# Optimization experiments

Hardware: AMD Instinct MI355X
Metric: run time of the kernel (lower is better)

The kernel has to match this reference:

```python
import jax, jax.numpy as jnp
import numpy as np
from jax import lax

IMG = 512            # image H = W
FH = FW = 32         # feature map spatial size
A = 9                # anchors per location (3 sizes x 3 ratios)
N = FH * FW * A      # total anchors = 9216
IOU_THR = 0.7
MIN_SCORE = 0.5
MIN_SIZE = 1e-3


def make_anchors():
    """Anchors in centroid format (cx, cy, w, h), ordered (H, W, A)."""
    stride = IMG / FH
    sizes = np.array([32.0, 64.0, 128.0])
    ratios = np.array([0.5, 1.0, 2.0])
    ws = (sizes[:, None] / np.sqrt(ratios)[None, :]).reshape(-1)  # (A,)
    hs = (sizes[:, None] * np.sqrt(ratios)[None, :]).reshape(-1)  # (A,)
    cx = (np.arange(FW) + 0.5) * stride
    cy = (np.arange(FH) + 0.5) * stride
    CX = np.broadcast_to(cx[None, :, None], (FH, FW, A))
    CY = np.broadcast_to(cy[:, None, None], (FH, FW, A))
    Wg = np.broadcast_to(ws[None, None, :], (FH, FW, A))
    Hg = np.broadcast_to(hs[None, None, :], (FH, FW, A))
    anc = np.stack([CX, CY, Wg, Hg], axis=-1).reshape(-1, 4)
    return jnp.asarray(anc, dtype=jnp.float32)


def pairwise_iou(b):
    # b: (N,4) corners x1,y1,x2,y2
    x1, y1, x2, y2 = b[:, 0], b[:, 1], b[:, 2], b[:, 3]
    area = (x2 - x1) * (y2 - y1)
    ix1 = jnp.maximum(x1[:, None], x1[None, :])
    iy1 = jnp.maximum(y1[:, None], y1[None, :])
    ix2 = jnp.minimum(x2[:, None], x2[None, :])
    iy2 = jnp.minimum(y2[:, None], y2[None, :])
    inter = jnp.maximum(ix2 - ix1, 0.0) * jnp.maximum(iy2 - iy1, 0.0)
    union = area[:, None] + area[None, :] - inter
    return inter / jnp.maximum(union, 1e-9)


def nms_keep(boxes, scores, valid):
    """Greedy NMS. Returns bool keep mask of shape (N,). Index decisions only."""
    s = jnp.where(valid, scores, -jnp.inf)
    order = jnp.argsort(-s)
    b = boxes[order]
    v = valid[order]
    ious = pairwise_iou(b)  # (N, N)
    idx = jnp.arange(N)

    def body(i, supp):
        keep_i = (~supp[i]) & v[i]
        return supp | (keep_i & (ious[i] > IOU_THR) & (idx > i))

    supp = lax.fori_loop(0, N, body, jnp.zeros(N, dtype=bool))
    keep_sorted = (~supp) & v
    return jnp.zeros(N, dtype=bool).at[order].set(keep_sorted)


def setup_inputs() -> dict:
    key = jax.random.key(0)
    ks = jax.random.split(key, 4)
    return {
        "feature_map": jax.random.normal(ks[0], (1, 256, FH, FW), jnp.float32),
        "conv1_w": jax.random.normal(ks[1], (512, 256, 3, 3), jnp.float32) * 0.02,
        "conv1_b": jnp.zeros((512,), jnp.float32),
        "conv2_w": jax.random.normal(ks[2], (A, 512), jnp.float32) * 0.01,
        "conv2_b": jnp.zeros((A,), jnp.float32),
        "conv3_w": jax.random.normal(ks[3], (4 * A, 512), jnp.float32) * 0.01,
        "conv3_b": jnp.zeros((4 * A,), jnp.float32),
    }


def reference(feature_map, conv1_w, conv1_b, conv2_w, conv2_b, conv3_w, conv3_b):
    anchors = make_anchors()  # (N,4) cx,cy,w,h

    # --- conv backbone head ---
    h = lax.conv_general_dilated(
        feature_map, conv1_w, (1, 1), "SAME",
        dimension_numbers=("NCHW", "OIHW", "NCHW"))
    h = jax.nn.relu(h + conv1_b[None, :, None, None])  # (1,512,H,W)

    scores = jax.nn.sigmoid(
        jnp.einsum("bchw,ac->bahw", h, conv2_w) + conv2_b[None, :, None, None])
    scores = scores.transpose(0, 2, 3, 1).reshape(-1)  # (N,) ordered (H,W,A)

    off = jnp.einsum("bchw,oc->bohw", h, conv3_w) + conv3_b[None, :, None, None]
    off = off.reshape(1, A, 4, FH, FW).transpose(0, 3, 4, 1, 2).reshape(-1, 4)

    acx, acy, aw, ah = anchors[:, 0], anchors[:, 1], anchors[:, 2], anchors[:, 3]
    cx = acx + off[:, 0] * aw
    cy = acy + off[:, 1] * ah
    bw = aw * jnp.exp(off[:, 2])
    bh = ah * jnp.exp(off[:, 3])
    boxes = jnp.stack([cx - bw / 2, cy - bh / 2, cx + bw / 2, cy + bh / 2], axis=1)

    # --- clip to image ---
    lo = jnp.array([0.0, 0.0, 0.0, 0.0], jnp.float32)
    hi = jnp.array([IMG, IMG, IMG, IMG], jnp.float32)
    boxes = jnp.clip(boxes, lo, hi)

    # --- remove small boxes + score threshold (as a mask, jit-safe) ---
    valid = ((boxes[:, 2] - boxes[:, 0]) >= MIN_SIZE) \
          & ((boxes[:, 3] - boxes[:, 1]) >= MIN_SIZE) \
          & (scores >= MIN_SCORE)

    # --- NMS (selection is index-based; no gradient through the decision) ---
    keep = nms_keep(lax.stop_gradient(boxes), lax.stop_gradient(scores), valid)

    out = jnp.concatenate(
        [boxes * keep[:, None].astype(boxes.dtype),
         (scores * keep.astype(scores.dtype))[:, None]], axis=1)  # (N,5)
    return out
```

## Files before the change

### kernel.cpp

```cpp
#include <hip/hip_runtime.h>
#include <math.h>

#define FHW   32
#define NA    9
#define NBOX  9216
#define C1    256
#define C2    512
#define KTOT  2304
#define KS    8
#define KCH   (KTOT / KS)
#define BK    16
#define NT    (KCH / BK)
#define CAP   64
#define ECAP  32768
#define ROUNDS 96

struct AnchorWH { float w[NA]; float h[NA]; };

#define FP_OFF    0u
#define WT_OFF    1183744u
#define HP_OFF    5902336u
#define BOX_OFF   22679552u
#define SC_OFF    22827008u
#define VL_OFF    22863872u
#define DEG_OFF   22900736u
#define ADJ_OFF   22937600u
#define NV_OFF    24117248u

__global__ __launch_bounds__(256) void k_prep(const float* __restrict__ fin,
                                              float* __restrict__ Fp,
                                              unsigned int* __restrict__ deg,
                                              unsigned int* __restrict__ nv,
                                              const float* __restrict__ w1,
                                              float* __restrict__ Wt,
                                              float* __restrict__ out) {
    if (blockIdx.x < 1156) {
        int idx = blockIdx.x * 256 + threadIdx.x;
        if (idx < 256 * 34 * 34) {
            int c   = idx / 1156;
            int rem = idx - c * 1156;
            int yy  = rem / 34;
            int xx  = rem - yy * 34;
            float v = 0.f;
            if (yy >= 1 && yy <= 32 && xx >= 1 && xx <= 32)
                v = fin[c * 1024 + (yy - 1) * 32 + (xx - 1)];
            Fp[idx] = v;
        }
        if (idx < NBOX)     deg[idx] = 0u;
        if (idx < NBOX * 5) out[idx] = 0.f;
        if (idx == 0)       *nv = 0u;
    } else {
        __shared__ float tile[32][33];
        int tb  = blockIdx.x - 1156;
        int k0  = (tb % 72) * 32;
        int oc0 = (tb / 72) * 32;
        int t   = threadIdx.x;
        int r0 = t >> 5, c = t & 31;
        #pragma unroll
        for (int i = 0; i < 4; ++i) {
            int r = r0 + 8 * i;
            tile[r][c] = w1[(oc0 + r) * KTOT + k0 + c];
        }
        __syncthreads();
        #pragma unroll
        for (int i = 0; i < 4; ++i) {
            int kk  = r0 + 8 * i;
            int k   = k0 + kk;
            int ch  = k / 9;
            int kap = k - ch * 9;
            Wt[(kap * 256 + ch) * C2 + oc0 + c] = tile[c][kk];
        }
    }
}

__global__ __launch_bounds__(256) void k_gemm(const float* __restrict__ Fp,
                                              const float* __restrict__ Wt,
                                              float* __restrict__ hp) {
    const int id = blockIdx.x;
    const int kz = id & 7;
    const int g  = id >> 3;
    const int by = g & 3, bx = g >> 2;
    const int p0  = bx * 128;
    const int oc0 = by * 128;
    const int k0b = kz * KCH;
    const int t  = threadIdx.x;
    const int ty = t >> 4, tx = t & 15;

    __shared__ float As[BK][128];
    __shared__ float Bs[BK][128];

    const int pp  = t & 127;
    const int th  = t >> 7;
    const int pyx = ((p0 + pp) >> 5) * 34 + ((p0 + pp) & 31);
    const int rB  = t >> 5;
    const int cB  = (t & 31) * 4;

    float acc[2][2][4][4];
    #pragma unroll
    for (int rh = 0; rh < 2; ++rh)
        #pragma unroll
        for (int ch = 0; ch < 2; ++ch)
            #pragma unroll
            for (int r = 0; r < 4; ++r)
                #pragma unroll
                for (int c = 0; c < 4; ++c) acc[rh][ch][r][c] = 0.f;

    float  aS[8];
    float4 bS0, bS1;

    auto LOAD = [&](int s) {
        int tap = s >> 8, c0 = s & 255;
        int dy  = (tap * 11) >> 5;
        int dx  = tap - 3 * dy;
        const float* ab = Fp + ((c0 + th) * 34 + dy) * 34 + dx + pyx;
        #pragma unroll
        for (int i = 0; i < 8; ++i) aS[i] = ab[i * 2312];
        const float* bb = Wt + (s + rB) * C2 + oc0 + cB;
        bS0 = *(const float4*)bb;
        bS1 = *(const float4*)(bb + 8 * C2);
    };
    auto STORE = [&]() {
        #pragma unroll
        for (int i = 0; i < 8; ++i) As[2 * i + th][pp] = aS[i];
        *(float4*)&Bs[rB][cB]     = bS0;
        *(float4*)&Bs[rB + 8][cB] = bS1;
    };

    LOAD(k0b);
    #pragma unroll 1
    for (int tile = 0; tile < NT; ++tile) {
        __syncthreads();
        STORE();
        __syncthreads();
        if (tile + 1 < NT) LOAD(k0b + (tile + 1) * BK);
        #pragma unroll
        for (int kk = 0; kk < BK; ++kk) {
            float a[2][4], b[2][4];
            *(float4*)&a[0][0] = *(const float4*)&As[kk][ty * 4];
            *(float4*)&a[1][0] = *(const float4*)&As[kk][ty * 4 + 64];
            *(float4*)&b[0][0] = *(const float4*)&Bs[kk][tx * 4];
            *(float4*)&b[1][0] = *(const float4*)&Bs[kk][tx * 4 + 64];
            #pragma unroll
            for (int rh = 0; rh < 2; ++rh)
                #pragma unroll
                for (int ch = 0; ch < 2; ++ch)
                    #pragma unroll
                    for (int r = 0; r < 4; ++r)
                        #pragma unroll
                        for (int c = 0; c < 4; ++c)
                            acc[rh][ch][r][c] = fmaf(a[rh][r], b[ch][c], acc[rh][ch][r][c]);
        }
    }

    #pragma unroll
    for (int rh = 0; rh < 2; ++rh)
        #pragma unroll
        for (int r = 0; r < 4; ++r) {
            int p = p0 + rh * 64 + ty * 4 + r;
            float* dst = hp + ((size_t)(kz * 1024 + p)) * C2 + oc0 + tx * 4;
            *(float4*)dst        = *(float4*)&acc[rh][0][r][0];
            *(float4*)(dst + 64) = *(float4*)&acc[rh][1][r][0];
        }
}

__global__ __launch_bounds__(256) void k_heads(const float* __restrict__ hp,
                                               const float* __restrict__ b1,
                                               const float* __restrict__ w2,
                                               const float* __restrict__ b2,
                                               const float* __restrict__ w3,
                                               const float* __restrict__ b3,
                                               float* __restrict__ boxes,
                                               float* __restrict__ scoresG,
                                               unsigned int* __restrict__ nv,
                                               unsigned int* __restrict__ vlist,
                                               AnchorWH awh) {
    const int p0 = blockIdx.x * 4;
    const int t  = threadIdx.x;
    __shared__ float hrow[4][C2];
    __shared__ float arr[4][45];

    #pragma unroll
    for (int px = 0; px < 4; ++px) {
        int p = p0 + px;
        #pragma unroll
        for (int i = 0; i < 2; ++i) {
            int c = t + 256 * i;
            float s = b1[c];
            #pragma unroll
            for (int ks = 0; ks < KS; ++ks) s += hp[((size_t)(ks * 1024 + p)) * C2 + c];
            hrow[px][c] = fmaxf(s, 0.f);
        }
    }
    __syncthreads();

    const int w = t >> 6, lane = t & 63;
    for (int job = w; job < 180; job += 4) {
        int px = job / 45, j = job - px * 45;
        const float* wp = (j < 9) ? (w2 + j * C2) : (w3 + (j - 9) * C2);
        float s = 0.f;
        #pragma unroll
        for (int i = 0; i < 8; ++i) s += hrow[px][lane + 64 * i] * wp[lane + 64 * i];
        #pragma unroll
        for (int d = 1; d < 64; d <<= 1) s += __shfl_xor(s, d, 64);
        if (lane == 0) arr[px][j] = s;
    }
    __syncthreads();

    if (t < 36) {
        int px = t / 9, a = t - px * 9;
        int p = p0 + px;
        float logit = arr[px][a] + b2[a];
        float score = 1.f / (1.f + expf(-logit));
        float o0 = arr[px][9 + a * 4 + 0] + b3[a * 4 + 0];
        float o1 = arr[px][9 + a * 4 + 1] + b3[a * 4 + 1];
        float o2 = arr[px][9 + a * 4 + 2] + b3[a * 4 + 2];
        float o3 = arr[px][9 + a * 4 + 3] + b3[a * 4 + 3];
        int y = p >> 5, x = p & 31;
        float ax = (x + 0.5f) * 16.f, ay = (y + 0.5f) * 16.f;
        float aw = awh.w[a], ah = awh.h[a];
        float cx = ax + o0 * aw;
        float cy = ay + o1 * ah;
        float bw = aw * expf(o2);
        float bh = ah * expf(o3);
        float x1 = fminf(fmaxf(cx - bw * 0.5f, 0.f), 512.f);
        float y1 = fminf(fmaxf(cy - bh * 0.5f, 0.f), 512.f);
        float x2 = fminf(fmaxf(cx + bw * 0.5f, 0.f), 512.f);
        float y2 = fminf(fmaxf(cy + bh * 0.5f, 0.f), 512.f);
        int n = p * 9 + a;
        float4 bx4; bx4.x = x1; bx4.y = y1; bx4.z = x2; bx4.w = y2;
        ((float4*)boxes)[n] = bx4;
        scoresG[n] = score;
        bool valid = (x2 - x1 >= 0.001f) && (y2 - y1 >= 0.001f) && (score >= 0.5f);
        if (valid) {
            unsigned int ci = atomicAdd(nv, 1u);
            vlist[ci] = (unsigned int)n;
        }
    }
}

__global__ __launch_bounds__(256) void k_adj(const unsigned int* __restrict__ nvp,
                                             const unsigned int* __restrict__ vlist,
                                             const float* __restrict__ boxes,
                                             const float* __restrict__ scoresG,
                                             unsigned int* __restrict__ deg,
                                             unsigned short* __restrict__ adj) {
    const int Nv = (int)*nvp;
    int b = blockIdx.x;
    int tv = (int)(sqrtf(2.f * b + 0.25f) - 0.5f);
    while ((tv + 1) * (tv + 2) / 2 <= b) tv++;
    while (tv * (tv + 1) / 2 > b) tv--;
    int tu = b - tv * (tv + 1) / 2;
    if (tv * 128 >= Nv) return;

    __shared__ float4 ub[128], vb[128];
    __shared__ float  us[128], vs[128];
    __shared__ int    uo[128], vo[128];
    int t = threadIdx.x;
    if (t < 128) {
        int gi = tu * 128 + t;
        if (gi < Nv) { int n = (int)vlist[gi]; ub[t] = ((const float4*)boxes)[n]; us[t] = scoresG[n]; uo[t] = n; }
        else us[t] = -1.f;
    } else {
        int tt = t - 128;
        int gj = tv * 128 + tt;
        if (gj < Nv) { int n = (int)vlist[gj]; vb[tt] = ((const float4*)boxes)[n]; vs[tt] = scoresG[n]; vo[tt] = n; }
        else vs[tt] = -1.f;
    }
    __syncthreads();

    for (int s = 0; s < 64; ++s) {
        int q  = t + 256 * s;
        int i  = q >> 7, jj = q & 127;
        if (tu == tv && i >= jj) continue;
        float su = us[i], sv = vs[jj];
        if (su < 0.f || sv < 0.f) continue;
        float4 bu = ub[i], bv = vb[jj];
        float au = (bu.z - bu.x) * (bu.w - bu.y);
        float av = (bv.z - bv.x) * (bv.w - bv.y);
        float ix1 = fmaxf(bu.x, bv.x), iy1 = fmaxf(bu.y, bv.y);
        float ix2 = fminf(bu.z, bv.z), iy2 = fminf(bu.w, bv.w);
        float inter = fmaxf(ix2 - ix1, 0.f) * fmaxf(iy2 - iy1, 0.f);
        float uni = au + av - inter;
        float iou = inter / fmaxf(uni, 1e-9f);
        if (iou > 0.7f) {
            int gi = tu * 128 + i, gj = tv * 128 + jj;
            bool uHigh = (su > sv) || (su == sv && uo[i] < vo[jj]);
            int lower = uHigh ? gj : gi;
            int upper = uHigh ? gi : gj;
            unsigned int slot = atomicAdd(&deg[lower], 1u);
            if (slot < CAP) adj[lower * CAP + slot] = (unsigned short)upper;
        }
    }
}

__global__ __launch_bounds__(512) void k_peel(const unsigned int* __restrict__ nvp,
                                              const unsigned int* __restrict__ vlist,
                                              const unsigned int* __restrict__ degG,
                                              const unsigned short* __restrict__ adjG,
                                              const float* __restrict__ boxes,
                                              const float* __restrict__ scoresG,
                                              float* __restrict__ out) {
    __shared__ unsigned short offL[NBOX + 2];
    __shared__ unsigned char  st[NBOX];
    __shared__ unsigned short csr[ECAP];
    __shared__ unsigned int   scratch[512];
    __shared__ unsigned char  flags[ROUNDS];
    const int t  = threadIdx.x;
    const int Nv = (int)*nvp;
    const int chunk = (Nv + 511) / 512;
    const int i0 = t * chunk;
    const int i1 = (i0 + chunk < Nv) ? (i0 + chunk) : Nv;

    if (t < ROUNDS) flags[t] = 0;

    unsigned int lsum = 0;
    for (int i = i0; i < i1; ++i) {
        unsigned int d = degG[i];
        if (d > CAP) d = CAP;
        st[i] = (unsigned char)d;
        lsum += d;
    }
    scratch[t] = lsum;
    __syncthreads();
    for (int ofs = 1; ofs < 512; ofs <<= 1) {
        unsigned int v = (t >= ofs) ? scratch[t - ofs] : 0u;
        __syncthreads();
        scratch[t] += v;
        __syncthreads();
    }
    if (t == 511) {
        unsigned int tot = scratch[511];
        offL[Nv] = (unsigned short)(tot < ECAP ? tot : ECAP);
    }
    unsigned int amask = 0;
    {
        unsigned int off = scratch[t] - lsum;
        for (int i = i0; i < i1; ++i) {
            unsigned int o = (off < ECAP) ? off : ECAP;
            offL[i] = (unsigned short)o;
            int d = st[i];
            int ld = (int)ECAP - (int)o; if (ld > d) ld = d; if (ld < 0) ld = 0;
            for (int s = 0; s < ld; ++s)
                csr[o + s] = adjG[i * CAP + s];
            off += d;
            if (d == 0) st[i] = 1;
            else { st[i] = 0; amask |= 1u << (i - i0); }
        }
    }
    __syncthreads();

    for (int r = 0; r < ROUNDS; ++r) {
        bool any = false;
        unsigned int m = amask;
        while (m) {
            int b = __ffs(m) - 1; m &= m - 1;
            int i = i0 + b;
            int o = offL[i], on = offL[i + 1];
            int d, ld;
            if (on < ECAP) { d = on - o; ld = d; }
            else {
                unsigned int dg = degG[i]; d = (dg > CAP) ? CAP : (int)dg;
                ld = (int)ECAP - o; if (ld < 0) ld = 0; if (ld > d) ld = d;
            }
            bool kseen = false, useen = false;
            for (int s = 0; s < d; ++s) {
                int j = (s < ld) ? (int)csr[o + s] : (int)adjG[i * CAP + s];
                unsigned char v = st[j];
                kseen |= (v == 1);
                useen |= (v == 0);
            }
            if (kseen)       { st[i] = 2; any = true; amask &= ~(1u << b); }
            else if (!useen) { st[i] = 1; any = true; amask &= ~(1u << b); }
        }
        if (any) flags[r] = 1;
        __syncthreads();
        if (!flags[r]) break;
    }

    for (int i = i0; i < i1; ++i) {
        if (st[i] == 1) {
            int n = (int)vlist[i];
            float4 b = ((const float4*)boxes)[n];
            out[n * 5 + 0] = b.x;
            out[n * 5 + 1] = b.y;
            out[n * 5 + 2] = b.z;
            out[n * 5 + 3] = b.w;
            out[n * 5 + 4] = scoresG[n];
        }
    }
}

extern "C" void kernel_launch(void* const* d_in, const int* in_sizes, int n_in,
                              void* d_out, int out_size, void* d_ws, size_t ws_size,
                              hipStream_t stream) {
    const float* fin = (const float*)d_in[0];
    const float* w1  = (const float*)d_in[1];
    const float* b1  = (const float*)d_in[2];
    const float* w2  = (const float*)d_in[3];
    const float* b2  = (const float*)d_in[4];
    const float* w3  = (const float*)d_in[5];
    const float* b3  = (const float*)d_in[6];
    float* out = (float*)d_out;

    char* ws = (char*)d_ws;
    float*          Fp    = (float*)(ws + FP_OFF);
    float*          Wt    = (float*)(ws + WT_OFF);
    float*          hp    = (float*)(ws + HP_OFF);
    float*          boxes = (float*)(ws + BOX_OFF);
    float*          sc    = (float*)(ws + SC_OFF);
    unsigned int*   vlist = (unsigned int*)(ws + VL_OFF);
    unsigned int*   deg   = (unsigned int*)(ws + DEG_OFF);
    unsigned short* adj   = (unsigned short*)(ws + ADJ_OFF);
    unsigned int*   nv    = (unsigned int*)(ws + NV_OFF);

    AnchorWH awh;
    {
        const double sizes[3]  = {32.0, 64.0, 128.0};
        const double ratios[3] = {0.5, 1.0, 2.0};
        for (int si = 0; si < 3; ++si)
            for (int ri = 0; ri < 3; ++ri) {
                awh.w[si * 3 + ri] = (float)(sizes[si] / sqrt(ratios[ri]));
                awh.h[si * 3 + ri] = (float)(sizes[si] * sqrt(ratios[ri]));
            }
    }

    k_prep<<<dim3(1156 + 72 * 16), 256, 0, stream>>>(fin, Fp, deg, nv, w1, Wt, out);
    k_gemm<<<dim3(256), 256, 0, stream>>>(Fp, Wt, hp);
    k_heads<<<dim3(256), 256, 0, stream>>>(hp, b1, w2, b2, w3, b3, boxes, sc, nv, vlist, awh);
    k_adj<<<dim3(72 * 73 / 2), 256, 0, stream>>>(nv, vlist, boxes, sc, deg, adj);
    k_peel<<<dim3(1), 512, 0, stream>>>(nv, vlist, deg, adj, boxes, sc, out);
}
```

Baseline: 207.5 us.

## Run NMS peeling rounds in a single wavefront to drop block barriers

```diff
diff --git a/kernel.cpp b/kernel.cpp
--- a/kernel.cpp
+++ b/kernel.cpp
@@ -13,7 +13,6 @@
 #define NT    (KCH / BK)
 #define CAP   64
 #define ECAP  32768
-#define ROUNDS 96
 
 struct AnchorWH { float w[NA]; float h[NA]; };
 
@@ -304,14 +303,11 @@
     __shared__ unsigned char  st[NBOX];
     __shared__ unsigned short csr[ECAP];
     __shared__ unsigned int   scratch[512];
-    __shared__ unsigned char  flags[ROUNDS];
     const int t  = threadIdx.x;
     const int Nv = (int)*nvp;
     const int chunk = (Nv + 511) / 512;
     const int i0 = t * chunk;
     const int i1 = (i0 + chunk < Nv) ? (i0 + chunk) : Nv;
-
-    if (t < ROUNDS) flags[t] = 0;
 
     unsigned int lsum = 0;
     for (int i = i0; i < i1; ++i) {
@@ -332,7 +328,6 @@
         unsigned int tot = scratch[511];
         offL[Nv] = (unsigned short)(tot < ECAP ? tot : ECAP);
     }
-    unsigned int amask = 0;
     {
         unsigned int off = scratch[t] - lsum;
         for (int i = i0; i < i1; ++i) {
@@ -343,39 +338,49 @@
             for (int s = 0; s < ld; ++s)
                 csr[o + s] = adjG[i * CAP + s];
             off += d;
-            if (d == 0) st[i] = 1;
-            else { st[i] = 0; amask |= 1u << (i - i0); }
-        }
-    }
-    __syncthreads();
-
-    for (int r = 0; r < ROUNDS; ++r) {
-        bool any = false;
-        unsigned int m = amask;
-        while (m) {
-            int b = __ffs(m) - 1; m &= m - 1;
-            int i = i0 + b;
-            int o = offL[i], on = offL[i + 1];
-            int d, ld;
-            if (on < ECAP) { d = on - o; ld = d; }
-            else {
-                unsigned int dg = degG[i]; d = (dg > CAP) ? CAP : (int)dg;
-                ld = (int)ECAP - o; if (ld < 0) ld = 0; if (ld > d) ld = d;
-            }
-            bool kseen = false, useen = false;
-            for (int s = 0; s < d; ++s) {
-                int j = (s < ld) ? (int)csr[o + s] : (int)adjG[i * CAP + s];
-                unsigned char v = st[j];
-                kseen |= (v == 1);
-                useen |= (v == 0);
-            }
-            if (kseen)       { st[i] = 2; any = true; amask &= ~(1u << b); }
-            else if (!useen) { st[i] = 1; any = true; amask &= ~(1u << b); }
-        }
-        if (any) flags[r] = 1;
-        __syncthreads();
-        if (!flags[r]) break;
-    }
+            st[i] = (d == 0) ? 1 : 0;
+        }
+    }
+    __syncthreads();
+
+    if (t < 64) {
+        unsigned long long m0 = 0ull, m1 = 0ull, m2 = 0ull;
+        for (int k = 0; k < 64; ++k) { int i = t + (k << 6);        if (i < Nv && st[i] == 0) m0 |= 1ull << k; }
+        for (int k = 0; k < 64; ++k) { int i = 4096 + t + (k << 6); if (i < Nv && st[i] == 0) m1 |= 1ull << k; }
+        for (int k = 0; k < 16; ++k) { int i = 8192 + t + (k << 6); if (i < Nv && st[i] == 0) m2 |= 1ull << k; }
+
+        for (int r = 0; r < 160; ++r) {
+            bool any = false;
+            auto SWEEP = [&](unsigned long long& m, int base) {
+                unsigned long long mm = m;
+                while (mm) {
+                    int b = __ffsll(mm) - 1; mm &= mm - 1;
+                    int i = base + t + (b << 6);
+                    int o = offL[i], on = offL[i + 1];
+                    int d, ld;
+                    if (on < ECAP) { d = on - o; ld = d; }
+                    else {
+                        unsigned int dg = degG[i]; d = (dg > CAP) ? CAP : (int)dg;
+                        ld = (int)ECAP - o; if (ld < 0) ld = 0; if (ld > d) ld = d;
+                    }
+                    bool kseen = false, useen = false;
+                    for (int s = 0; s < d; ++s) {
+                        int j = (s < ld) ? (int)csr[o + s] : (int)adjG[i * CAP + s];
+                        unsigned char v = st[j];
+                        kseen |= (v == 1);
+                        useen |= (v == 0);
+                    }
+                    if (kseen)       { st[i] = 2; any = true; m &= ~(1ull << b); }
+                    else if (!useen) { st[i] = 1; any = true; m &= ~(1ull << b); }
+                }
+            };
+            SWEEP(m0, 0); SWEEP(m1, 4096); SWEEP(m2, 8192);
+            if (!__any(any)) break;
+            asm volatile("s_waitcnt lgkmcnt(0)" ::: "memory");
+            __builtin_amdgcn_sched_barrier(0);
+        }
+    }
+    __syncthreads();
 
     for (int i = i0; i < i1; ++i) {
         if (st[i] == 1) {
```

Measured after the change: 241.9 us. 16.6% more time.
